# Kernel optimization log

Hardware: AMD Instinct MI355X
Metric: run time of the kernel (lower is better)

## Reference

```python
import jax, jax.numpy as jnp
import numpy as np

N_NODES = 100000
N_EDGES = 800000
IN_CH, HID_CH, OUT_CH = 128, 256, 128


def setup_inputs() -> dict:
    key = jax.random.key(0)
    ks = jax.random.split(key, 8)
    x = jax.random.normal(ks[0], (N_NODES, IN_CH), dtype=jnp.float32)
    edge_index = jax.random.randint(ks[1], (2, N_EDGES), 0, N_NODES, dtype=jnp.int64)
    def lin(k, fan_in, fan_out):
        bound = 1.0 / np.sqrt(fan_in)
        return jax.random.uniform(k, (fan_out, fan_in), minval=-bound, maxval=bound, dtype=jnp.float32)
    # PyG SAGEConv: lin_l (neighbor branch, with bias), lin_r (root branch, no bias)
    W1l = lin(ks[2], IN_CH, HID_CH)
    b1l = jnp.zeros((HID_CH,), dtype=jnp.float32)
    W1r = lin(ks[3], IN_CH, HID_CH)
    W2l = lin(ks[4], HID_CH, OUT_CH)
    b2l = jnp.zeros((OUT_CH,), dtype=jnp.float32)
    W2r = lin(ks[5], HID_CH, OUT_CH)
    return {"x": x, "edge_index": edge_index, "W1l": W1l, "b1l": b1l, "W1r": W1r,
            "W2l": W2l, "b2l": b2l, "W2r": W2r}


def _sage_conv(x, src, dst, Wl, bl, Wr):
    # mean-aggregate messages x[src] at dst, then lin_l(agg) + lin_r(x)
    msgs = x[src]                                        # [E, C]
    summed = jax.ops.segment_sum(msgs, dst, num_segments=N_NODES)
    cnt = jax.ops.segment_sum(jnp.ones((src.shape[0],), dtype=x.dtype), dst, num_segments=N_NODES)
    mean = summed / jnp.maximum(cnt, 1.0)[:, None]       # [N, C]
    return mean @ Wl.T + bl + x @ Wr.T


def reference(x, edge_index, W1l, b1l, W1r, W2l, b2l, W2r):
    src, dst = edge_index[0], edge_index[1]
    h = _sage_conv(x, src, dst, W1l, b1l, W1r)
    h = jax.nn.relu(h)
    # dropout is identity in eval mode (F.dropout with training=False)
    out = _sage_conv(h, src, dst, W2l, b2l, W2r)
    return out
```

## Files before the change

### kernel.cpp

```cpp
#include <hip/hip_runtime.h>

#define N_NODES 100000
#define N_EDGES 800000
#define SCAN_CHUNK 1024
#define SCAN_NB ((N_NODES + SCAN_CHUNK - 1) / SCAN_CHUNK)

typedef __attribute__((ext_vector_type(8))) _Float16 f16x8;
typedef __attribute__((ext_vector_type(4))) _Float16 f16x4;
typedef __attribute__((ext_vector_type(4))) float f32x4;

__global__ void count_int_k(const int* __restrict__ dst, int* __restrict__ cnt, int E) {
    int i = blockIdx.x * blockDim.x + threadIdx.x;
    if (i < E) atomicAdd(&cnt[dst[i]], 1);
}

__global__ __launch_bounds__(256) void scan1_k(const int* __restrict__ cnt,
                                               int* __restrict__ offs,
                                               int* __restrict__ bsums, int N) {
    __shared__ int s[256];
    int t = threadIdx.x;
    int base = blockIdx.x * SCAN_CHUNK + t * 4;
    int v0 = (base + 0 < N) ? cnt[base + 0] : 0;
    int v1 = (base + 1 < N) ? cnt[base + 1] : 0;
    int v2 = (base + 2 < N) ? cnt[base + 2] : 0;
    int v3 = (base + 3 < N) ? cnt[base + 3] : 0;
    int tsum = v0 + v1 + v2 + v3;
    s[t] = tsum;
    __syncthreads();
    for (int off = 1; off < 256; off <<= 1) {
        int val = (t >= off) ? s[t - off] : 0;
        __syncthreads();
        s[t] += val;
        __syncthreads();
    }
    int excl = s[t] - tsum;
    if (base + 0 < N) offs[base + 0] = excl;
    if (base + 1 < N) offs[base + 1] = excl + v0;
    if (base + 2 < N) offs[base + 2] = excl + v0 + v1;
    if (base + 3 < N) offs[base + 3] = excl + v0 + v1 + v2;
    if (t == 255) bsums[blockIdx.x] = s[255];
}

__global__ __launch_bounds__(256) void scan2_k(const int* __restrict__ bsums,
                                               int* __restrict__ boffs, int nb) {
    __shared__ int s[256];
    int t = threadIdx.x;
    int v = (t < nb) ? bsums[t] : 0;
    s[t] = v;
    __syncthreads();
    for (int off = 1; off < 256; off <<= 1) {
        int val = (t >= off) ? s[t - off] : 0;
        __syncthreads();
        s[t] += val;
        __syncthreads();
    }
    if (t < nb) boffs[t] = s[t] - v;
}

__global__ void scan3_k(int* __restrict__ offs, int* __restrict__ cursor,
                        const int* __restrict__ boffs, int N, int E) {
    int i = blockIdx.x * blockDim.x + threadIdx.x;
    if (i < N) {
        int v = offs[i] + boffs[i >> 10];
        offs[i] = v;
        cursor[i] = v;
    }
    if (i == 0) offs[N] = E;
}

__global__ void fill_k(const int* __restrict__ src, const int* __restrict__ dst,
                       int* __restrict__ cursor, int* __restrict__ perm, int E) {
    int e = blockIdx.x * blockDim.x + threadIdx.x;
    if (e < E) {
        int d = dst[e];
        int slot = atomicAdd(&cursor[d], 1);
        perm[slot] = src[e];
    }
}

__global__ __launch_bounds__(256) void cvt_f16_k(const float* __restrict__ in,
                                                 _Float16* __restrict__ outp, int n8) {
    int i = blockIdx.x * blockDim.x + threadIdx.x;
    if (i >= n8) return;
    const float4* p = (const float4*)in + (long long)i * 2;
    float4 v0 = p[0], v1 = p[1];
    f16x8 h;
    h[0] = (_Float16)v0.x; h[1] = (_Float16)v0.y;
    h[2] = (_Float16)v0.z; h[3] = (_Float16)v0.w;
    h[4] = (_Float16)v1.x; h[5] = (_Float16)v1.y;
    h[6] = (_Float16)v1.z; h[7] = (_Float16)v1.w;
    *(f16x8*)&outp[(long long)i * 8] = h;
}

__global__ __launch_bounds__(256) void aggmean_k(const _Float16* __restrict__ feat16,
                                                 const int* __restrict__ perm,
                                                 const int* __restrict__ offs,
                                                 _Float16* __restrict__ m16, int N) {
    int tid = threadIdx.x;
    int node = blockIdx.x * 16 + (tid >> 4);
    int q = tid & 15;
    if (node >= N) return;
    int beg = offs[node], end = offs[node + 1];
    float a[8], b[8];
#pragma unroll
    for (int k = 0; k < 8; k++) { a[k] = 0.0f; b[k] = 0.0f; }
    int i = beg;
    for (; i + 1 < end; i += 2) {
        f16x8 v0 = *(const f16x8*)&feat16[(long long)perm[i] * 128 + q * 8];
        f16x8 v1 = *(const f16x8*)&feat16[(long long)perm[i + 1] * 128 + q * 8];
#pragma unroll
        for (int k = 0; k < 8; k++) { a[k] += (float)v0[k]; b[k] += (float)v1[k]; }
    }
    if (i < end) {
        f16x8 v0 = *(const f16x8*)&feat16[(long long)perm[i] * 128 + q * 8];
#pragma unroll
        for (int k = 0; k < 8; k++) a[k] += (float)v0[k];
    }
    float rc = 1.0f / fmaxf((float)(end - beg), 1.0f);
    f16x8 v;
#pragma unroll
    for (int k = 0; k < 8; k++) v[k] = (_Float16)((a[k] + b[k]) * rc);
    *(f16x8*)&m16[(long long)node * 128 + q * 8] = v;
}

__global__ __launch_bounds__(256) void aggout_k(const _Float16* __restrict__ g16,
                                                const int* __restrict__ perm,
                                                const int* __restrict__ offs,
                                                const _Float16* __restrict__ r2h,
                                                const float* __restrict__ b2l,
                                                float* __restrict__ out, int N) {
    int tid = threadIdx.x;
    int node = blockIdx.x * 16 + (tid >> 4);
    int q = tid & 15;
    if (node >= N) return;
    int beg = offs[node], end = offs[node + 1];
    float a[8], b[8];
#pragma unroll
    for (int k = 0; k < 8; k++) { a[k] = 0.0f; b[k] = 0.0f; }
    int i = beg;
    for (; i + 1 < end; i += 2) {
        f16x8 v0 = *(const f16x8*)&g16[(long long)perm[i] * 128 + q * 8];
        f16x8 v1 = *(const f16x8*)&g16[(long long)perm[i + 1] * 128 + q * 8];
#pragma unroll
        for (int k = 0; k < 8; k++) { a[k] += (float)v0[k]; b[k] += (float)v1[k]; }
    }
    if (i < end) {
        f16x8 v0 = *(const f16x8*)&g16[(long long)perm[i] * 128 + q * 8];
#pragma unroll
        for (int k = 0; k < 8; k++) a[k] += (float)v0[k];
    }
    float rc = 1.0f / fmaxf((float)(end - beg), 1.0f);
    f16x8 rv = *(const f16x8*)&r2h[(long long)node * 128 + q * 8];
    float4 bv0 = ((const float4*)b2l)[q * 2];
    float4 bv1 = ((const float4*)b2l)[q * 2 + 1];
    float4 o0, o1;
    o0.x = (a[0] + b[0]) * rc + (float)rv[0] + bv0.x;
    o0.y = (a[1] + b[1]) * rc + (float)rv[1] + bv0.y;
    o0.z = (a[2] + b[2]) * rc + (float)rv[2] + bv0.z;
    o0.w = (a[3] + b[3]) * rc + (float)rv[3] + bv0.w;
    o1.x = (a[4] + b[4]) * rc + (float)rv[4] + bv1.x;
    o1.y = (a[5] + b[5]) * rc + (float)rv[5] + bv1.y;
    o1.z = (a[6] + b[6]) * rc + (float)rv[6] + bv1.z;
    o1.w = (a[7] + b[7]) * rc + (float)rv[7] + bv1.w;
    ((float4*)out)[(long long)node * 32 + q * 2]     = o0;
    ((float4*)out)[(long long)node * 32 + q * 2 + 1] = o1;
}

__device__ inline void gload16(const void* g, void* l) {
    __builtin_amdgcn_global_load_lds(
        (const __attribute__((address_space(1))) unsigned int*)g,
        (__attribute__((address_space(3))) unsigned int*)l,
        16, 0, 0);
}

template <int LAYER>
__global__ __launch_bounds__(1024, 4) void gemm_mfma_k(
        const _Float16* __restrict__ Ap0, const _Float16* __restrict__ Ap1,
        const _Float16* __restrict__ Bp0, const _Float16* __restrict__ Bp1,
        const float* __restrict__ bias,
        _Float16* __restrict__ O1h,
        _Float16* __restrict__ OH, int N) {
    __shared__ _Float16 As[256 * 128];
    __shared__ _Float16 Bs[256 * 128];

    const int m0 = blockIdx.x * 256;
    const int tid = threadIdx.x;
    const int lane = tid & 63;
    const int wid = tid >> 6;
    const int wm = wid >> 2, wn = wid & 3;
    const int lr = lane & 15, lg = lane >> 4;

    const int r4 = lane >> 4;
    const int scs = lane & 15;

    f32x4 acc[4][4];
#pragma unroll
    for (int i = 0; i < 4; i++)
#pragma unroll
        for (int j = 0; j < 4; j++) acc[i][j] = (f32x4)0.0f;

#pragma unroll
    for (int kt = 0; kt < 2; ++kt) {
        __syncthreads();
        {
            const _Float16* Asrc;
            int aoffk;
            if constexpr (LAYER == 1) { Asrc = kt ? Ap1 : Ap0; aoffk = 0; }
            else                      { Asrc = Ap0;            aoffk = kt * 128; }
            constexpr int RSA = (LAYER == 1) ? 128 : 256;
#pragma unroll
            for (int it = 0; it < 4; ++it) {
                int seg = wid * 4 + it;
                int row = seg * 4 + r4;
                int k16 = scs ^ (row & 15);
                int gn = m0 + row;
                if (gn < N)
                    gload16(Asrc + (long long)gn * RSA + aoffk + k16 * 8, &As[seg * 512]);
            }
#pragma unroll
            for (int it = 0; it < 4; ++it) {
                int seg = wid * 4 + it;
                int row = seg * 4 + r4;
                int k16 = scs ^ (row & 15);
                const _Float16* Bsrc;
                long long boff;
                if constexpr (LAYER == 1) {
                    Bsrc = kt ? Bp1 : Bp0;
                    boff = (long long)row * 128;
                } else {
                    Bsrc = (row < 128) ? Bp0 : Bp1;
                    boff = (long long)(row & 127) * 256 + kt * 128;
                }
                gload16(Bsrc + boff + k16 * 8, &Bs[seg * 512]);
            }
        }
        __syncthreads();

#pragma unroll
        for (int ks = 0; ks < 4; ++ks) {
            const int c = ks * 4 + lg;
            f16x8 bf[4];
#pragma unroll
            for (int fc = 0; fc < 4; ++fc) {
                int c_ = wn * 64 + fc * 16 + lr;
                bf[fc] = *(const f16x8*)&Bs[c_ * 128 + (c ^ (c_ & 15)) * 8];
            }
#pragma unroll
            for (int fr = 0; fr < 4; ++fr) {
                int r_ = wm * 64 + fr * 16 + lr;
                f16x8 af = *(const f16x8*)&As[r_ * 128 + (c ^ (r_ & 15)) * 8];
#pragma unroll
                for (int fc = 0; fc < 4; ++fc)
                    acc[fr][fc] = __builtin_amdgcn_mfma_f32_16x16x32_f16(af, bf[fc], acc[fr][fc], 0, 0, 0);
            }
        }
    }

    if constexpr (LAYER == 1) {
#pragma unroll
        for (int fc = 0; fc < 4; ++fc) {
            int col = wn * 64 + fc * 16 + lr;
            float bv = bias[col];
#pragma unroll
            for (int fr = 0; fr < 4; ++fr) {
#pragma unroll
                for (int j = 0; j < 4; ++j) {
                    int row = m0 + wm * 64 + fr * 16 + lg * 4 + j;
                    if (row < N)
                        OH[(long long)row * 256 + col] =
                            (_Float16)fmaxf(acc[fr][fc][j] + bv, 0.0f);
                }
            }
        }
    } else {
#pragma unroll
        for (int fc = 0; fc < 4; ++fc) {
            int col = wn * 64 + fc * 16 + lr;
            _Float16* dp = (col < 128) ? OH : O1h;
            int dcol = col & 127;
#pragma unroll
            for (int fr = 0; fr < 4; ++fr) {
#pragma unroll
                for (int j = 0; j < 4; ++j) {
                    int row = m0 + wm * 64 + fr * 16 + lg * 4 + j;
                    if (row < N)
                        dp[(long long)row * 128 + dcol] = (_Float16)acc[fr][fc][j];
                }
            }
        }
    }
}

extern "C" void kernel_launch(void* const* d_in, const int* in_sizes, int n_in,
                              void* d_out, int out_size, void* d_ws, size_t ws_size,
                              hipStream_t stream) {
    const float* x   = (const float*)d_in[0];
    const int*   ei  = (const int*)d_in[1];
    const float* W1l = (const float*)d_in[2];
    const float* b1l = (const float*)d_in[3];
    const float* W1r = (const float*)d_in[4];
    const float* W2l = (const float*)d_in[5];
    const float* b2l = (const float*)d_in[6];
    const float* W2r = (const float*)d_in[7];
    float* out = (float*)d_out;

    const int N = N_NODES, E = N_EDGES;
    const int* srcI = ei;
    const int* dstI = ei + E;

    char* ws = (char*)d_ws;
    size_t off = 0;
    auto alloc = [&](size_t bytes) {
        size_t o = off;
        off += (bytes + 511) & ~(size_t)511;
        return o;
    };
    size_t off_cnt   = alloc((size_t)N * 4);
    size_t off_offs  = alloc((size_t)(N + 1) * 4);
    size_t off_cur   = alloc((size_t)N * 4);
    size_t off_bsum  = alloc((size_t)SCAN_NB * 4);
    size_t off_boff  = alloc((size_t)SCAN_NB * 4);
    size_t off_perm  = alloc((size_t)E * 4);
    size_t off_x16   = alloc((size_t)N * 128 * 2);
    size_t off_m16   = alloc((size_t)N * 128 * 2);
    size_t off_h16   = alloc((size_t)N * 256 * 2);
    size_t off_g16   = alloc((size_t)N * 128 * 2);
    size_t off_r2    = alloc((size_t)N * 128 * 2);
    size_t off_w     = alloc((size_t)4 * 32768 * 2);
    int*      cntI = (int*)(ws + off_cnt);
    int*      offs = (int*)(ws + off_offs);
    int*      cur  = (int*)(ws + off_cur);
    int*      bsum = (int*)(ws + off_bsum);
    int*      boff = (int*)(ws + off_boff);
    int*      perm = (int*)(ws + off_perm);
    _Float16* x16  = (_Float16*)(ws + off_x16);
    _Float16* m16  = (_Float16*)(ws + off_m16);
    _Float16* h16  = (_Float16*)(ws + off_h16);
    _Float16* g16  = (_Float16*)(ws + off_g16);
    _Float16* r2h  = (_Float16*)(ws + off_r2);
    _Float16* wbuf = (_Float16*)(ws + off_w);
    const int WSZ = 32768;
    _Float16* w1l16 = wbuf;            _Float16* w1r16 = wbuf + WSZ;
    _Float16* w2l16 = wbuf + 2 * WSZ;  _Float16* w2r16 = wbuf + 3 * WSZ;

    (void)hipMemsetAsync(cntI, 0, (size_t)N * 4, stream);
    count_int_k<<<(E + 255) / 256, 256, 0, stream>>>(dstI, cntI, E);
    scan1_k<<<SCAN_NB, 256, 0, stream>>>(cntI, offs, bsum, N);
    scan2_k<<<1, 256, 0, stream>>>(bsum, boff, SCAN_NB);
    scan3_k<<<(N + 255) / 256, 256, 0, stream>>>(offs, cur, boff, N, E);
    fill_k<<<(E + 255) / 256, 256, 0, stream>>>(srcI, dstI, cur, perm, E);

    {
        int n8x = N * 16;
        cvt_f16_k<<<(n8x + 255) / 256, 256, 0, stream>>>(x, x16, n8x);
        int n8w = 32768 / 8;
        cvt_f16_k<<<(n8w + 255) / 256, 256, 0, stream>>>(W1l, w1l16, n8w);
        cvt_f16_k<<<(n8w + 255) / 256, 256, 0, stream>>>(W1r, w1r16, n8w);
        cvt_f16_k<<<(n8w + 255) / 256, 256, 0, stream>>>(W2l, w2l16, n8w);
        cvt_f16_k<<<(n8w + 255) / 256, 256, 0, stream>>>(W2r, w2r16, n8w);
    }

    aggmean_k<<<(N + 15) / 16, 256, 0, stream>>>(x16, perm, offs, m16, N);
    {
        int nblk = (N + 255) / 256;
        gemm_mfma_k<1><<<nblk, 1024, 0, stream>>>(m16, x16, w1l16, w1r16,
                                                  b1l, nullptr, h16, N);
    }

    {
        int nblk = (N + 255) / 256;
        gemm_mfma_k<2><<<nblk, 1024, 0, stream>>>(h16, h16, w2l16, w2r16,
                                                  nullptr, r2h, g16, N);
    }
    aggout_k<<<(N + 15) / 16, 256, 0, stream>>>(g16, perm, offs, r2h, b2l, out, N);
}
```

Before: 279.4 us.

## Replace tiled GEMM with persistent streaming GEMM keeping full weights in LDS

The two SAGE GEMMs now run as persistent kernels with 256 blocks of 512 threads. Each block loads the whole 256x256 fp16 weight matrix into LDS once, then streams 16-row A tiles through a double buffer with async global-to-LDS loads. This removes the per-tile reloading of the weights and tries to overlap A loads with MFMA work. The trade-off is only 16-row tiles per step, one block per CU, a barrier every tile, and low MFMA work per wave, so latency may dominate.

New measurement: 276.1 us. Within noise of the previous version (-1.2%).

```diff
diff --git a/kernel.cpp b/kernel.cpp
--- a/kernel.cpp
+++ b/kernel.cpp
@@ -4,6 +4,8 @@
 #define N_EDGES 800000
 #define SCAN_CHUNK 1024
 #define SCAN_NB ((N_NODES + SCAN_CHUNK - 1) / SCAN_CHUNK)
+#define ROWS_PER_BLK 391
+#define TILES 25
 
 typedef __attribute__((ext_vector_type(8))) _Float16 f16x8;
 typedef __attribute__((ext_vector_type(4))) _Float16 f16x4;
@@ -174,120 +176,117 @@
 }
 
 template <int LAYER>
-__global__ __launch_bounds__(1024, 4) void gemm_mfma_k(
+__global__ __launch_bounds__(512, 1) void gemm_stream_k(
         const _Float16* __restrict__ Ap0, const _Float16* __restrict__ Ap1,
         const _Float16* __restrict__ Bp0, const _Float16* __restrict__ Bp1,
         const float* __restrict__ bias,
         _Float16* __restrict__ O1h,
         _Float16* __restrict__ OH, int N) {
-    __shared__ _Float16 As[256 * 128];
-    __shared__ _Float16 Bs[256 * 128];
-
-    const int m0 = blockIdx.x * 256;
+    __shared__ _Float16 Bs[256 * 256];
+    __shared__ _Float16 As2[2][16 * 256];
+
+    const int mbase = blockIdx.x * ROWS_PER_BLK;
+    const int rend = min(mbase + ROWS_PER_BLK, N);
     const int tid = threadIdx.x;
     const int lane = tid & 63;
     const int wid = tid >> 6;
-    const int wm = wid >> 2, wn = wid & 3;
     const int lr = lane & 15, lg = lane >> 4;
-
-    const int r4 = lane >> 4;
-    const int scs = lane & 15;
-
-    f32x4 acc[4][4];
-#pragma unroll
-    for (int i = 0; i < 4; i++)
-#pragma unroll
-        for (int j = 0; j < 4; j++) acc[i][j] = (f32x4)0.0f;
-
-#pragma unroll
-    for (int kt = 0; kt < 2; ++kt) {
-        __syncthreads();
-        {
-            const _Float16* Asrc;
-            int aoffk;
-            if constexpr (LAYER == 1) { Asrc = kt ? Ap1 : Ap0; aoffk = 0; }
-            else                      { Asrc = Ap0;            aoffk = kt * 128; }
-            constexpr int RSA = (LAYER == 1) ? 128 : 256;
-#pragma unroll
-            for (int it = 0; it < 4; ++it) {
-                int seg = wid * 4 + it;
-                int row = seg * 4 + r4;
-                int k16 = scs ^ (row & 15);
-                int gn = m0 + row;
-                if (gn < N)
-                    gload16(Asrc + (long long)gn * RSA + aoffk + k16 * 8, &As[seg * 512]);
+    const int r2 = lane >> 5;
+    const int scs = lane & 31;
+
+#pragma unroll
+    for (int it = 0; it < 16; ++it) {
+        int seg = wid * 16 + it;
+        int col = seg * 2 + r2;
+        int ck = scs ^ (col & 15);
+        const _Float16* src;
+        if constexpr (LAYER == 1)
+            src = (ck < 16) ? (Bp0 + (long long)col * 128 + ck * 8)
+                            : (Bp1 + (long long)col * 128 + (ck - 16) * 8);
+        else
+            src = (col < 128) ? (Bp0 + (long long)col * 256 + ck * 8)
+                              : (Bp1 + (long long)(col - 128) * 256 + ck * 8);
+        gload16(src, &Bs[seg * 512]);
+    }
+    {
+        int lrow = wid * 2 + r2;
+        int ck = scs ^ (lrow & 15);
+        int gn = mbase + lrow;
+        if (gn < N) {
+            const _Float16* src;
+            if constexpr (LAYER == 1)
+                src = (ck < 16) ? (Ap0 + (long long)gn * 128 + ck * 8)
+                                : (Ap1 + (long long)gn * 128 + (ck - 16) * 8);
+            else
+                src = Ap0 + (long long)gn * 256 + ck * 8;
+            gload16(src, &As2[0][wid * 512]);
+        }
+    }
+    asm volatile("s_waitcnt vmcnt(0)" ::: "memory");
+    __builtin_amdgcn_s_barrier();
+
+#pragma unroll 1
+    for (int t = 0; t < TILES; ++t) {
+        if (t + 1 < TILES) {
+            int lrow = wid * 2 + r2;
+            int ck = scs ^ (lrow & 15);
+            int gn = mbase + (t + 1) * 16 + lrow;
+            if (gn < N) {
+                const _Float16* src;
+                if constexpr (LAYER == 1)
+                    src = (ck < 16) ? (Ap0 + (long long)gn * 128 + ck * 8)
+                                    : (Ap1 + (long long)gn * 128 + (ck - 16) * 8);
+                else
+                    src = Ap0 + (long long)gn * 256 + ck * 8;
+                gload16(src, &As2[(t + 1) & 1][wid * 512]);
             }
-#pragma unroll
-            for (int it = 0; it < 4; ++it) {
-                int seg = wid * 4 + it;
-                int row = seg * 4 + r4;
-                int k16 = scs ^ (row & 15);
-                const _Float16* Bsrc;
-                long long boff;
-                if constexpr (LAYER == 1) {
-                    Bsrc = kt ? Bp1 : Bp0;
-                    boff = (long long)row * 128;
-                } else {
-                    Bsrc = (row < 128) ? Bp0 : Bp1;
-                    boff = (long long)(row & 127) * 256 + kt * 128;
-                }
-                gload16(Bsrc + boff + k16 * 8, &Bs[seg * 512]);
+            asm volatile("s_waitcnt vmcnt(1)" ::: "memory");
+        } else {
+            asm volatile("s_waitcnt vmcnt(0)" ::: "memory");
+        }
+        __builtin_amdgcn_sched_barrier(0);
+        __builtin_amdgcn_s_barrier();
+
+        const _Float16* Ab = &As2[t & 1][0];
+        f32x4 acc[2];
+        acc[0] = (f32x4)0.0f;
+        acc[1] = (f32x4)0.0f;
+#pragma unroll
+        for (int ks = 0; ks < 8; ++ks) {
+            int c = ks * 4 + lg;
+            f16x8 af = *(const f16x8*)&Ab[lr * 256 + (c ^ lr) * 8];
+#pragma unroll
+            for (int fc = 0; fc < 2; ++fc) {
+                int col = wid * 32 + fc * 16 + lr;
+                f16x8 bf = *(const f16x8*)&Bs[col * 256 + (c ^ (col & 15)) * 8];
+                acc[fc] = __builtin_amdgcn_mfma_f32_16x16x32_f16(af, bf, acc[fc], 0, 0, 0);
             }
         }
-        __syncthreads();
-
-#pragma unroll
-        for (int ks = 0; ks < 4; ++ks) {
-            const int c = ks * 4 + lg;
-            f16x8 bf[4];
-#pragma unroll
-            for (int fc = 0; fc < 4; ++fc) {
-                int c_ = wn * 64 + fc * 16 + lr;
-                bf[fc] = *(const f16x8*)&Bs[c_ * 128 + (c ^ (c_ & 15)) * 8];
-            }
-#pragma unroll
-            for (int fr = 0; fr < 4; ++fr) {
-                int r_ = wm * 64 + fr * 16 + lr;
-                f16x8 af = *(const f16x8*)&As[r_ * 128 + (c ^ (r_ & 15)) * 8];
-#pragma unroll
-                for (int fc = 0; fc < 4; ++fc)
-                    acc[fr][fc] = __builtin_amdgcn_mfma_f32_16x16x32_f16(af, bf[fc], acc[fr][fc], 0, 0, 0);
-            }
-        }
-    }
-
-    if constexpr (LAYER == 1) {
-#pragma unroll
-        for (int fc = 0; fc < 4; ++fc) {
-            int col = wn * 64 + fc * 16 + lr;
-            float bv = bias[col];
-#pragma unroll
-            for (int fr = 0; fr < 4; ++fr) {
+
+#pragma unroll
+        for (int fc = 0; fc < 2; ++fc) {
+            int col = wid * 32 + fc * 16 + lr;
+            if constexpr (LAYER == 1) {
+                float bv = bias[col];
 #pragma unroll
                 for (int j = 0; j < 4; ++j) {
-                    int row = m0 + wm * 64 + fr * 16 + lg * 4 + j;
-                    if (row < N)
+                    int row = mbase + t * 16 + lg * 4 + j;
+                    if (row < rend)
                         OH[(long long)row * 256 + col] =
-                            (_Float16)fmaxf(acc[fr][fc][j] + bv, 0.0f);
+                            (_Float16)fmaxf(acc[fc][j] + bv, 0.0f);
+                }
+            } else {
+                _Float16* dp = (col < 128) ? OH : O1h;
+                int dcol = col & 127;
+#pragma unroll
+                for (int j = 0; j < 4; ++j) {
+                    int row = mbase + t * 16 + lg * 4 + j;
+                    if (row < rend)
+                        dp[(long long)row * 128 + dcol] = (_Float16)acc[fc][j];
                 }
             }
         }
-    } else {
-#pragma unroll
-        for (int fc = 0; fc < 4; ++fc) {
-            int col = wn * 64 + fc * 16 + lr;
-            _Float16* dp = (col < 128) ? OH : O1h;
-            int dcol = col & 127;
-#pragma unroll
-            for (int fr = 0; fr < 4; ++fr) {
-#pragma unroll
-                for (int j = 0; j < 4; ++j) {
-                    int row = m0 + wm * 64 + fr * 16 + lg * 4 + j;
-                    if (row < N)
-                        dp[(long long)row * 128 + dcol] = (_Float16)acc[fr][fc][j];
-                }
-            }
-        }
+        __builtin_amdgcn_s_barrier();
     }
 }
 
@@ -361,16 +360,10 @@
     }
 
     aggmean_k<<<(N + 15) / 16, 256, 0, stream>>>(x16, perm, offs, m16, N);
-    {
-        int nblk = (N + 255) / 256;
-        gemm_mfma_k<1><<<nblk, 1024, 0, stream>>>(m16, x16, w1l16, w1r16,
-                                                  b1l, nullptr, h16, N);
-    }
-
-    {
-        int nblk = (N + 255) / 256;
-        gemm_mfma_k<2><<<nblk, 1024, 0, stream>>>(h16, h16, w2l16, w2r16,
-                                                  nullptr, r2h, g16, N);
-    }
+    gemm_stream_k<1><<<256, 512, 0, stream>>>(m16, x16, w1l16, w1r16,
+                                              b1l, nullptr, h16, N);
+
+    gemm_stream_k<2><<<256, 512, 0, stream>>>(h16, h16, w2l16, w2r16,
+                                              nullptr, r2h, g16, N);
     aggout_k<<<(N + 15) / 16, 256, 0, stream>>>(g16, perm, offs, r2h, b2l, out, N);
 }
```
